# Kernel optimization log

Measured on AMD Instinct MI355X. Metric: run time of the kernel, lower is better.

## Reference

```python
import jax, jax.numpy as jnp
import numpy as np

N = 100000
E = 1600000
IN_DIM, HID, OUT = 512, 128, 16


def setup_inputs() -> dict:
    key = jax.random.key(0)
    ks = jax.random.split(key, 8)
    x = jax.random.normal(ks[0], (N, IN_DIM), dtype=jnp.float32)
    edge_index = jax.random.randint(ks[1], (2, E), 0, N, dtype=jnp.int64)
    # GCNConv params (Glorot-ish scale) and Linear head
    W1 = jax.random.normal(ks[2], (IN_DIM, HID), dtype=jnp.float32) / np.sqrt(IN_DIM)
    b1 = jnp.zeros((HID,), dtype=jnp.float32)
    W2 = jax.random.normal(ks[3], (HID, HID), dtype=jnp.float32) / np.sqrt(HID)
    b2 = jnp.zeros((HID,), dtype=jnp.float32)
    Wl = jax.random.normal(ks[4], (HID, OUT), dtype=jnp.float32) / np.sqrt(HID)
    bl = jnp.zeros((OUT,), dtype=jnp.float32)
    return {"x": x, "edge_index": edge_index, "W1": W1, "b1": b1,
            "W2": W2, "b2": b2, "Wl": Wl, "bl": bl}


def _gcn_conv(x, W, b, src, dst, deg_inv_sqrt, deg_inv):
    # h = x @ W ; out[dst] += norm * h[src]; self-loop adds h[i]/deg[i]
    h = x @ W                                           # [N, D]
    norm = deg_inv_sqrt[src] * deg_inv_sqrt[dst]        # [E]
    msgs = h[src] * norm[:, None]                       # [E, D] gather
    agg = jax.ops.segment_sum(msgs, dst, num_segments=x.shape[0])  # scatter
    agg = agg + h * deg_inv[:, None]                    # self-loop term
    return agg + b


def reference(x, edge_index, W1, b1, W2, b2, Wl, bl):
    src, dst = edge_index[0], edge_index[1]
    n = x.shape[0]
    ones = jnp.ones(src.shape[0], dtype=x.dtype)
    # degree with self-loops (PyG gcn_norm counts in-degree at target + 1)
    deg = jax.ops.segment_sum(ones, dst, num_segments=n) + 1.0
    deg_inv_sqrt = jax.lax.rsqrt(deg)
    deg_inv = 1.0 / deg

    h = _gcn_conv(x, W1, b1, src, dst, deg_inv_sqrt, deg_inv)
    h = jax.nn.relu(h)
    # dropout: inference mode (training=False) -> identity
    h = _gcn_conv(h, W2, b2, src, dst, deg_inv_sqrt, deg_inv)
    embeddings = jax.nn.relu(h)
    out = embeddings @ Wl + bl
    return out, embeddings
```

## Files before the change

### kernel.cpp

```cpp
#include <hip/hip_runtime.h>

#define NN 100000
#define EE 1600000
#define IND 512
#define HIDD 128
#define OUTD 16
#define DEG_BLKS 128
#define GEMM_BLKS 782

typedef __bf16 bf16x8 __attribute__((ext_vector_type(8)));
typedef float f32x4 __attribute__((ext_vector_type(4)));

__device__ __forceinline__ ushort f2bf(float f) {
    union { float f; uint u; } v; v.f = f;
    uint r = v.u + 0x7FFFu + ((v.u >> 16) & 1u);
    return (ushort)(r >> 16);
}

__device__ __forceinline__ uint pk2bf(float a, float b) {
    __bf16 x = (__bf16)a, y = (__bf16)b;
    ushort ux = *(ushort*)&x, uy = *(ushort*)&y;
    return (uint)ux | ((uint)uy << 16);
}

#define GLDS16(src, dst)                                              \
    __builtin_amdgcn_global_load_lds(                                 \
        (const __attribute__((address_space(1))) void*)(src),         \
        (__attribute__((address_space(3))) void*)(dst), 16, 0, 0)

__global__ void k_prep(const float* __restrict__ W1, const float* __restrict__ W2,
                       ushort* __restrict__ Wt1, ushort* __restrict__ Wt2) {
    int b = blockIdx.x, tid = threadIdx.x;
    if (b < 256) {
        int i = b * 256 + tid;
        int k = i >> 7, n = i & 127;
        Wt1[n * 512 + k] = f2bf(W1[i]);
    } else {
        int i = (b - 256) * 256 + tid;
        int k = i >> 7, n = i & 127;
        Wt2[n * 128 + k] = f2bf(W2[i]);
    }
}

__global__ void k_scan_local(const int* __restrict__ deg, int* __restrict__ incl,
                             int* __restrict__ bsum) {
    __shared__ int s[256];
    int tid = threadIdx.x;
    int i = blockIdx.x * 256 + tid;
    int v = (i < NN) ? deg[i] : 0;
    s[tid] = v;
    __syncthreads();
    for (int off = 1; off < 256; off <<= 1) {
        int t = (tid >= off) ? s[tid - off] : 0;
        __syncthreads();
        s[tid] += t;
        __syncthreads();
    }
    if (i < NN) incl[i] = s[tid];
    if (tid == 255) bsum[blockIdx.x] = s[255];
}

__global__ void k_scan_bsum(const int* __restrict__ bsum, int* __restrict__ boff, int n) {
    __shared__ int s[512];
    int tid = threadIdx.x;
    int v = (tid < n) ? bsum[tid] : 0;
    s[tid] = v;
    __syncthreads();
    for (int off = 1; off < 512; off <<= 1) {
        int t = (tid >= off) ? s[tid - off] : 0;
        __syncthreads();
        s[tid] += t;
        __syncthreads();
    }
    if (tid < n) boff[tid] = s[tid] - v;
}

__global__ void k_scan_final(const int* __restrict__ incl, const int* __restrict__ deg,
                             const int* __restrict__ boff, int* __restrict__ rs,
                             int* __restrict__ cursor, float* __restrict__ dis,
                             float* __restrict__ dinv) {
    int i = blockIdx.x * 256 + threadIdx.x;
    if (i < NN) {
        int d = deg[i];
        int v = incl[i] + boff[i >> 8];
        int start = v - d;
        rs[i] = start;
        cursor[i] = start;
        if (i == NN - 1) rs[NN] = v;
        float df = (float)(d + 1);
        dis[i] = rsqrtf(df);
        dinv[i] = 1.0f / df;
    }
}

__global__ void k_fill(const int* __restrict__ src, const int* __restrict__ dst,
                       const float* __restrict__ dis, int* __restrict__ cursor,
                       int2* __restrict__ ew) {
    int i = blockIdx.x * blockDim.x + threadIdx.x;
    int stride = gridDim.x * blockDim.x;
    for (; i < EE; i += stride) {
        int d = dst[i];
        int s = src[i];
        int pos = atomicAdd(&cursor[d], 1);
        ew[pos] = make_int2(s, __float_as_int(dis[s] * dis[d]));
    }
}

template <int K, bool AFP32>
__device__ __forceinline__ void gemm_body(const void* __restrict__ Ap,
                                          const ushort* __restrict__ Wt,
                                          ushort* __restrict__ C, int M, int blk) {
    constexpr int NT = K / 32;
    constexpr int ABYTES = AFP32 ? 128 * 32 * 4 : 128 * 32 * 2;
    constexpr int WBYTES = 128 * 32 * 2;
    __shared__ char smem[2 * (ABYTES + WBYTES)];

    int tid = threadIdx.x;
    int row0 = blk * 128;
    int wid = tid >> 6, lane = tid & 63;
    int wm = wid * 32;
    int lm = lane & 15, lk8 = (lane >> 4) * 8;

    const float* Af = (const float*)Ap;
    const ushort* Ab16 = (const ushort*)Ap;

    f32x4 acc[8][2];
#pragma unroll
    for (int q = 0; q < 8; q++)
#pragma unroll
        for (int r = 0; r < 2; r++) acc[q][r] = (f32x4){0.f, 0.f, 0.f, 0.f};

    auto stage = [&](int bi, int k0) {
        char* Abase = smem + bi * ABYTES;
        char* Wbase = smem + 2 * ABYTES + bi * WBYTES;
        if (AFP32) {
#pragma unroll
            for (int j = 0; j < 4; j++) {
                int c = wid * 4 + j;
                int rp = c * 8 + (lane >> 3);
                int sl = (lane & 7) ^ (rp & 7);
                int gr2 = row0 + rp; if (gr2 >= M) gr2 = M - 1;
                GLDS16(Af + (size_t)gr2 * K + k0 + sl * 4, Abase + c * 1024);
            }
        } else {
#pragma unroll
            for (int j = 0; j < 2; j++) {
                int c = wid * 2 + j;
                int rp = c * 16 + (lane >> 2);
                int sl = (lane & 3) ^ (rp & 3);
                int gr2 = row0 + rp; if (gr2 >= M) gr2 = M - 1;
                GLDS16(Ab16 + (size_t)gr2 * K + k0 + sl * 8, Abase + c * 1024);
            }
        }
#pragma unroll
        for (int j = 0; j < 2; j++) {
            int c = wid * 2 + j;
            int rp = c * 16 + (lane >> 2);
            int sl = (lane & 3) ^ (rp & 3);
            GLDS16(Wt + (size_t)rp * K + k0 + sl * 8, Wbase + c * 1024);
        }
    };

    stage(0, 0);

    int cur = 0;
    for (int t = 0; t < NT; t++) {
        if (t + 1 < NT) {
            stage((t + 1) & 1, (t + 1) * 32);
            if (AFP32) asm volatile("s_waitcnt vmcnt(6)" ::: "memory");
            else       asm volatile("s_waitcnt vmcnt(4)" ::: "memory");
        } else {
            asm volatile("s_waitcnt vmcnt(0)" ::: "memory");
        }
        __builtin_amdgcn_s_barrier();

        char* Abase = smem + cur * ABYTES;
        char* Wbase = smem + 2 * ABYTES + cur * WBYTES;
        bf16x8 xf[2], wf[8];
        if (AFP32) {
#pragma unroll
            for (int r = 0; r < 2; r++) {
                int r_ = wm + r * 16 + lm;
                int s0 = lk8 >> 2;
                f32x4 a0 = *(const f32x4*)(Abase + r_ * 128 + (((s0)     ^ (r_ & 7)) << 4));
                f32x4 a1 = *(const f32x4*)(Abase + r_ * 128 + (((s0 + 1) ^ (r_ & 7)) << 4));
                uint4 u;
                u.x = pk2bf(a0[0], a0[1]);
                u.y = pk2bf(a0[2], a0[3]);
                u.z = pk2bf(a1[0], a1[1]);
                u.w = pk2bf(a1[2], a1[3]);
                xf[r] = *(bf16x8*)&u;
            }
        } else {
#pragma unroll
            for (int r = 0; r < 2; r++) {
                int r_ = wm + r * 16 + lm;
                int s = lk8 >> 3;
                uint4 u = *(const uint4*)(Abase + r_ * 64 + ((s ^ (r_ & 3)) << 4));
                xf[r] = *(bf16x8*)&u;
            }
        }
#pragma unroll
        for (int q = 0; q < 8; q++) {
            int n_ = q * 16 + lm;
            int s = lk8 >> 3;
            uint4 u = *(const uint4*)(Wbase + n_ * 64 + ((s ^ (n_ & 3)) << 4));
            wf[q] = *(bf16x8*)&u;
        }
#pragma unroll
        for (int q = 0; q < 8; q++)
#pragma unroll
            for (int r = 0; r < 2; r++)
                acc[q][r] = __builtin_amdgcn_mfma_f32_16x16x32_bf16(wf[q], xf[r], acc[q][r], 0, 0, 0);

        asm volatile("" ::: "memory");
        __builtin_amdgcn_s_barrier();
        cur ^= 1;
    }

    int cn4 = (lane >> 4) * 4;
#pragma unroll
    for (int r = 0; r < 2; r++) {
        int m = row0 + wm + r * 16 + lm;
        if (m < M) {
#pragma unroll
            for (int q = 0; q < 8; q++) {
                int n = q * 16 + cn4;
                uint2 o;
                o.x = (uint)f2bf(acc[q][r][0]) | ((uint)f2bf(acc[q][r][1]) << 16);
                o.y = (uint)f2bf(acc[q][r][2]) | ((uint)f2bf(acc[q][r][3]) << 16);
                *(uint2*)(C + (size_t)m * 128 + n) = o;
            }
        }
    }
}

__global__ __launch_bounds__(256) void k_mega1(const float* __restrict__ x,
                                               const ushort* __restrict__ Wt1,
                                               ushort* __restrict__ C,
                                               const int* __restrict__ dst,
                                               int* __restrict__ deg) {
    if (blockIdx.x < DEG_BLKS) {
        int i = blockIdx.x * 256 + threadIdx.x;
        int stride = DEG_BLKS * 256;
        for (; i < EE; i += stride) atomicAdd(&deg[dst[i]], 1);
    } else {
        gemm_body<IND, true>(x, Wt1, C, NN, blockIdx.x - DEG_BLKS);
    }
}

__global__ __launch_bounds__(256) void k_gemm2(const ushort* __restrict__ A,
                                               const ushort* __restrict__ Wt,
                                               ushort* __restrict__ C) {
    gemm_body<HIDD, false>(A, Wt, C, NN, blockIdx.x);
}

template <bool OUTF32>
__global__ __launch_bounds__(256) void k_agg(const ushort* __restrict__ h,
                                             const int* __restrict__ rs,
                                             const int2* __restrict__ ew,
                                             const float* __restrict__ dinv,
                                             const float* __restrict__ bias,
                                             void* __restrict__ yv) {
    int node = blockIdx.x * 4 + (threadIdx.x >> 6);
    int lane = threadIdx.x & 63;
    if (node >= NN) return;
    int half = lane >> 5, c = lane & 31;
    const uint2* h64 = (const uint2*)h;

    float acc0 = 0.f, acc1 = 0.f, acc2 = 0.f, acc3 = 0.f;
    if (half == 0) {
        float dv = dinv[node];
        uint2 sv = h64[(size_t)node * 32 + c];
        acc0 = __uint_as_float(sv.x << 16) * dv;
        acc1 = __uint_as_float(sv.x & 0xffff0000u) * dv;
        acc2 = __uint_as_float(sv.y << 16) * dv;
        acc3 = __uint_as_float(sv.y & 0xffff0000u) * dv;
    }

    int e = rs[node], e1 = rs[node + 1];

#define EL(i) int2 p##i = ew[e + 2 * i + half]; \
              uint2 g##i = h64[(size_t)(uint)p##i.x * 32 + c];
#define EA(i) { float w##i = __int_as_float(p##i.y); \
    acc0 += w##i * __uint_as_float(g##i.x << 16); \
    acc1 += w##i * __uint_as_float(g##i.x & 0xffff0000u); \
    acc2 += w##i * __uint_as_float(g##i.y << 16); \
    acc3 += w##i * __uint_as_float(g##i.y & 0xffff0000u); }

    for (; e + 16 <= e1; e += 16) {
        EL(0) EL(1) EL(2) EL(3) EL(4) EL(5) EL(6) EL(7)
        EA(0) EA(1) EA(2) EA(3) EA(4) EA(5) EA(6) EA(7)
    }
    for (; e + 4 <= e1; e += 4) {
        EL(0) EL(1)
        EA(0) EA(1)
    }
    if (e + 2 <= e1) {
        EL(0)
        EA(0)
        e += 2;
    }
    if (e < e1 && half == 0) {
        int2 p = ew[e];
        uint2 g = h64[(size_t)(uint)p.x * 32 + c];
        float w = __int_as_float(p.y);
        acc0 += w * __uint_as_float(g.x << 16);
        acc1 += w * __uint_as_float(g.x & 0xffff0000u);
        acc2 += w * __uint_as_float(g.y << 16);
        acc3 += w * __uint_as_float(g.y & 0xffff0000u);
    }
#undef EL
#undef EA

    acc0 += __shfl_xor(acc0, 32, 64);
    acc1 += __shfl_xor(acc1, 32, 64);
    acc2 += __shfl_xor(acc2, 32, 64);
    acc3 += __shfl_xor(acc3, 32, 64);

    if (half == 0) {
        float4 bv = *(const float4*)(bias + c * 4);
        acc0 = fmaxf(acc0 + bv.x, 0.f);
        acc1 = fmaxf(acc1 + bv.y, 0.f);
        acc2 = fmaxf(acc2 + bv.z, 0.f);
        acc3 = fmaxf(acc3 + bv.w, 0.f);
        if (OUTF32) {
            *(float4*)((float*)yv + (size_t)node * 128 + c * 4) =
                make_float4(acc0, acc1, acc2, acc3);
        } else {
            uint2 o;
            o.x = (uint)f2bf(acc0) | ((uint)f2bf(acc1) << 16);
            o.y = (uint)f2bf(acc2) | ((uint)f2bf(acc3) << 16);
            *(uint2*)((ushort*)yv + (size_t)node * 128 + c * 4) = o;
        }
    }
}

__global__ __launch_bounds__(256) void k_out(const float* __restrict__ emb,
                                             const float* __restrict__ Wl,
                                             const float* __restrict__ bl,
                                             float* __restrict__ out) {
    __shared__ float wl_s[128 * 16];
    __shared__ float es[16][129];
    int tid = threadIdx.x;
    int row0 = blockIdx.x * 16;
#pragma unroll
    for (int p = 0; p < 8; p++) wl_s[p * 256 + tid] = Wl[p * 256 + tid];
#pragma unroll
    for (int p = 0; p < 8; p++) {
        int idx = p * 256 + tid;
        int r = idx >> 7, c = idx & 127;
        int gr = row0 + r;
        es[r][c] = (gr < NN) ? emb[(size_t)gr * 128 + c] : 0.0f;
    }
    __syncthreads();
    int r = tid >> 4, o = tid & 15;
    float acc = bl[o];
#pragma unroll
    for (int k = 0; k < 128; k++) acc += es[r][k] * wl_s[k * 16 + o];
    int gr = row0 + r;
    if (gr < NN) out[(size_t)gr * 16 + o] = acc;
}

extern "C" void kernel_launch(void* const* d_in, const int* in_sizes, int n_in,
                              void* d_out, int out_size, void* d_ws, size_t ws_size,
                              hipStream_t stream) {
    const float* x  = (const float*)d_in[0];
    const int* ei   = (const int*)d_in[1];
    const float* W1 = (const float*)d_in[2];
    const float* b1 = (const float*)d_in[3];
    const float* W2 = (const float*)d_in[4];
    const float* b2 = (const float*)d_in[5];
    const float* Wl = (const float*)d_in[6];
    const float* bl = (const float*)d_in[7];
    const int* src = ei;
    const int* dst = ei + EE;

    float* outp = (float*)d_out;
    float* emb  = outp + (size_t)NN * OUTD;

    int2* ew    = (int2*)d_ws;
    ushort* h_a = (ushort*)(ew + EE);
    ushort* h_b = h_a + (size_t)NN * 128;
    ushort* Wt1 = h_b + (size_t)NN * 128;
    ushort* Wt2 = Wt1 + 128 * 512;
    int* deg    = (int*)(Wt2 + 128 * 128);
    float* dis  = (float*)(deg + NN);
    float* dinv = dis + NN;
    int* incl   = (int*)(dinv + NN);
    int* rs     = incl + NN;
    int* cursor = rs + NN + 8;
    int* bsum   = cursor + NN;
    int* boff   = bsum + 512;

    const int NB_N = (NN + 255) / 256;

    hipMemsetAsync(deg, 0, (size_t)NN * sizeof(int), stream);
    k_prep<<<320, 256, 0, stream>>>(W1, W2, Wt1, Wt2);
    k_mega1<<<DEG_BLKS + GEMM_BLKS, 256, 0, stream>>>(x, Wt1, h_a, dst, deg);
    k_scan_local<<<NB_N, 256, 0, stream>>>(deg, incl, bsum);
    k_scan_bsum<<<1, 512, 0, stream>>>(bsum, boff, NB_N);
    k_scan_final<<<NB_N, 256, 0, stream>>>(incl, deg, boff, rs, cursor, dis, dinv);
    k_fill<<<2048, 256, 0, stream>>>(src, dst, dis, cursor, ew);

    k_agg<false><<<(NN + 3) / 4, 256, 0, stream>>>(h_a, rs, ew, dinv, b1, h_b);
    k_gemm2<<<GEMM_BLKS, 256, 0, stream>>>(h_b, Wt2, h_a);
    k_agg<true><<<(NN + 3) / 4, 256, 0, stream>>>(h_a, rs, ew, dinv, b2, emb);
    k_out<<<(NN + 15) / 16, 256, 0, stream>>>(emb, Wl, bl, outp);
}
```

Measured before the change: 376.8 us.

## Halve GEMM row tile to 64 and raise occupancy via launch bounds

Shrinks the GEMM block tile from 128 to 64 rows, so each wave computes one 16-row MFMA slice instead of two. The grid doubles, the accumulator registers halve, and LDS per block drops; launch bounds now request more blocks per CU for both GEMM kernels. The aim is more latency hiding and better load balance across CUs for this memory-bound GEMM. In exchange, the W tile is reloaded twice as often per output row and each block issues fewer MFMAs per barrier.

```diff
diff --git a/kernel.cpp b/kernel.cpp
--- a/kernel.cpp
+++ b/kernel.cpp
@@ -6,7 +6,7 @@
 #define HIDD 128
 #define OUTD 16
 #define DEG_BLKS 128
-#define GEMM_BLKS 782
+#define GEMM_BLKS 1563
 
 typedef __bf16 bf16x8 __attribute__((ext_vector_type(8)));
 typedef float f32x4 __attribute__((ext_vector_type(4)));
@@ -111,46 +111,41 @@
                                           const ushort* __restrict__ Wt,
                                           ushort* __restrict__ C, int M, int blk) {
     constexpr int NT = K / 32;
-    constexpr int ABYTES = AFP32 ? 128 * 32 * 4 : 128 * 32 * 2;
+    constexpr int ABYTES = AFP32 ? 64 * 32 * 4 : 64 * 32 * 2;
     constexpr int WBYTES = 128 * 32 * 2;
     __shared__ char smem[2 * (ABYTES + WBYTES)];
 
     int tid = threadIdx.x;
-    int row0 = blk * 128;
+    int row0 = blk * 64;
     int wid = tid >> 6, lane = tid & 63;
-    int wm = wid * 32;
+    int wm = wid * 16;
     int lm = lane & 15, lk8 = (lane >> 4) * 8;
 
     const float* Af = (const float*)Ap;
     const ushort* Ab16 = (const ushort*)Ap;
 
-    f32x4 acc[8][2];
-#pragma unroll
-    for (int q = 0; q < 8; q++)
-#pragma unroll
-        for (int r = 0; r < 2; r++) acc[q][r] = (f32x4){0.f, 0.f, 0.f, 0.f};
+    f32x4 acc[8];
+#pragma unroll
+    for (int q = 0; q < 8; q++) acc[q] = (f32x4){0.f, 0.f, 0.f, 0.f};
 
     auto stage = [&](int bi, int k0) {
         char* Abase = smem + bi * ABYTES;
         char* Wbase = smem + 2 * ABYTES + bi * WBYTES;
         if (AFP32) {
 #pragma unroll
-            for (int j = 0; j < 4; j++) {
-                int c = wid * 4 + j;
+            for (int j = 0; j < 2; j++) {
+                int c = wid * 2 + j;
                 int rp = c * 8 + (lane >> 3);
                 int sl = (lane & 7) ^ (rp & 7);
                 int gr2 = row0 + rp; if (gr2 >= M) gr2 = M - 1;
                 GLDS16(Af + (size_t)gr2 * K + k0 + sl * 4, Abase + c * 1024);
             }
         } else {
-#pragma unroll
-            for (int j = 0; j < 2; j++) {
-                int c = wid * 2 + j;
-                int rp = c * 16 + (lane >> 2);
-                int sl = (lane & 3) ^ (rp & 3);
-                int gr2 = row0 + rp; if (gr2 >= M) gr2 = M - 1;
-                GLDS16(Ab16 + (size_t)gr2 * K + k0 + sl * 8, Abase + c * 1024);
-            }
+            int c = wid;
+            int rp = c * 16 + (lane >> 2);
+            int sl = (lane & 3) ^ (rp & 3);
+            int gr2 = row0 + rp; if (gr2 >= M) gr2 = M - 1;
+            GLDS16(Ab16 + (size_t)gr2 * K + k0 + sl * 8, Abase + c * 1024);
         }
 #pragma unroll
         for (int j = 0; j < 2; j++) {
@@ -167,8 +162,8 @@
     for (int t = 0; t < NT; t++) {
         if (t + 1 < NT) {
             stage((t + 1) & 1, (t + 1) * 32);
-            if (AFP32) asm volatile("s_waitcnt vmcnt(6)" ::: "memory");
-            else       asm volatile("s_waitcnt vmcnt(4)" ::: "memory");
+            if (AFP32) asm volatile("s_waitcnt vmcnt(4)" ::: "memory");
+            else       asm volatile("s_waitcnt vmcnt(3)" ::: "memory");
         } else {
             asm volatile("s_waitcnt vmcnt(0)" ::: "memory");
         }
@@ -176,29 +171,23 @@
 
         char* Abase = smem + cur * ABYTES;
         char* Wbase = smem + 2 * ABYTES + cur * WBYTES;
-        bf16x8 xf[2], wf[8];
+        bf16x8 xf, wf[8];
         if (AFP32) {
-#pragma unroll
-            for (int r = 0; r < 2; r++) {
-                int r_ = wm + r * 16 + lm;
-                int s0 = lk8 >> 2;
-                f32x4 a0 = *(const f32x4*)(Abase + r_ * 128 + (((s0)     ^ (r_ & 7)) << 4));
-                f32x4 a1 = *(const f32x4*)(Abase + r_ * 128 + (((s0 + 1) ^ (r_ & 7)) << 4));
-                uint4 u;
-                u.x = pk2bf(a0[0], a0[1]);
-                u.y = pk2bf(a0[2], a0[3]);
-                u.z = pk2bf(a1[0], a1[1]);
-                u.w = pk2bf(a1[2], a1[3]);
-                xf[r] = *(bf16x8*)&u;
-            }
+            int r_ = wm + lm;
+            int s0 = lk8 >> 2;
+            f32x4 a0 = *(const f32x4*)(Abase + r_ * 128 + (((s0)     ^ (r_ & 7)) << 4));
+            f32x4 a1 = *(const f32x4*)(Abase + r_ * 128 + (((s0 + 1) ^ (r_ & 7)) << 4));
+            uint4 u;
+            u.x = pk2bf(a0[0], a0[1]);
+            u.y = pk2bf(a0[2], a0[3]);
+            u.z = pk2bf(a1[0], a1[1]);
+            u.w = pk2bf(a1[2], a1[3]);
+            xf = *(bf16x8*)&u;
         } else {
-#pragma unroll
-            for (int r = 0; r < 2; r++) {
-                int r_ = wm + r * 16 + lm;
-                int s = lk8 >> 3;
-                uint4 u = *(const uint4*)(Abase + r_ * 64 + ((s ^ (r_ & 3)) << 4));
-                xf[r] = *(bf16x8*)&u;
-            }
+            int r_ = wm + lm;
+            int s = lk8 >> 3;
+            uint4 u = *(const uint4*)(Abase + r_ * 64 + ((s ^ (r_ & 3)) << 4));
+            xf = *(bf16x8*)&u;
         }
 #pragma unroll
         for (int q = 0; q < 8; q++) {
@@ -209,9 +198,7 @@
         }
 #pragma unroll
         for (int q = 0; q < 8; q++)
-#pragma unroll
-            for (int r = 0; r < 2; r++)
-                acc[q][r] = __builtin_amdgcn_mfma_f32_16x16x32_bf16(wf[q], xf[r], acc[q][r], 0, 0, 0);
+            acc[q] = __builtin_amdgcn_mfma_f32_16x16x32_bf16(wf[q], xf, acc[q], 0, 0, 0);
 
         asm volatile("" ::: "memory");
         __builtin_amdgcn_s_barrier();
@@ -219,27 +206,24 @@
     }
 
     int cn4 = (lane >> 4) * 4;
-#pragma unroll
-    for (int r = 0; r < 2; r++) {
-        int m = row0 + wm + r * 16 + lm;
-        if (m < M) {
-#pragma unroll
-            for (int q = 0; q < 8; q++) {
-                int n = q * 16 + cn4;
-                uint2 o;
-                o.x = (uint)f2bf(acc[q][r][0]) | ((uint)f2bf(acc[q][r][1]) << 16);
-                o.y = (uint)f2bf(acc[q][r][2]) | ((uint)f2bf(acc[q][r][3]) << 16);
-                *(uint2*)(C + (size_t)m * 128 + n) = o;
-            }
-        }
-    }
-}
-
-__global__ __launch_bounds__(256) void k_mega1(const float* __restrict__ x,
-                                               const ushort* __restrict__ Wt1,
-                                               ushort* __restrict__ C,
-                                               const int* __restrict__ dst,
-                                               int* __restrict__ deg) {
+    int m = row0 + wm + lm;
+    if (m < M) {
+#pragma unroll
+        for (int q = 0; q < 8; q++) {
+            int n = q * 16 + cn4;
+            uint2 o;
+            o.x = (uint)f2bf(acc[q][0]) | ((uint)f2bf(acc[q][1]) << 16);
+            o.y = (uint)f2bf(acc[q][2]) | ((uint)f2bf(acc[q][3]) << 16);
+            *(uint2*)(C + (size_t)m * 128 + n) = o;
+        }
+    }
+}
+
+__global__ __launch_bounds__(256, 5) void k_mega1(const float* __restrict__ x,
+                                                  const ushort* __restrict__ Wt1,
+                                                  ushort* __restrict__ C,
+                                                  const int* __restrict__ dst,
+                                                  int* __restrict__ deg) {
     if (blockIdx.x < DEG_BLKS) {
         int i = blockIdx.x * 256 + threadIdx.x;
         int stride = DEG_BLKS * 256;
@@ -249,9 +233,9 @@
     }
 }
 
-__global__ __launch_bounds__(256) void k_gemm2(const ushort* __restrict__ A,
-                                               const ushort* __restrict__ Wt,
-                                               ushort* __restrict__ C) {
+__global__ __launch_bounds__(256, 6) void k_gemm2(const ushort* __restrict__ A,
+                                                  const ushort* __restrict__ Wt,
+                                                  ushort* __restrict__ C) {
     gemm_body<HIDD, false>(A, Wt, C, NN, blockIdx.x);
 }
 
```

New measurement: 374.2 us. No clear change (-0.7%).
